# Kernel optimization log

Measured on AMD Instinct MI355X. Metric: run time of the kernel, lower is better.

Reference implementation:

```python
import jax, jax.numpy as jnp
import numpy as np


def _bilinear_resize_nchw(x, out_h, out_w):
    """Torch F.interpolate(mode='bilinear', align_corners=False), no antialias."""
    B, C, H, W = x.shape

    def coords(out_n, in_n):
        src = jnp.maximum(0.0, (jnp.arange(out_n, dtype=jnp.float32) + 0.5) * (in_n / out_n) - 0.5)
        f = jnp.floor(src)
        i0 = jnp.clip(f.astype(jnp.int32), 0, in_n - 1)
        i1 = jnp.clip(i0 + 1, 0, in_n - 1)
        frac = src - f
        return i0, i1, frac

    y0, y1, fy = coords(out_h, H)
    x0, x1, fx = coords(out_w, W)
    rows = x[:, :, y0, :] * (1.0 - fy)[None, None, :, None] + x[:, :, y1, :] * fy[None, None, :, None]
    out = rows[:, :, :, x0] * (1.0 - fx)[None, None, None, :] + rows[:, :, :, x1] * fx[None, None, None, :]
    return out


def setup_inputs() -> dict:
    key = jax.random.key(0)
    k1, k2, k3, k4 = jax.random.split(key, 4)
    return {
        "query_value": jax.random.normal(k1, (2, 256, 64, 128), dtype=jnp.float32),
        "memory_keys_low": jax.random.normal(k2, (2, 4, 64, 32, 64), dtype=jnp.float32),
        "memory_values_low": jax.random.normal(k3, (2, 4, 256, 32, 64), dtype=jnp.float32),
        "query_key_low": jax.random.normal(k4, (2, 64, 32, 64), dtype=jnp.float32),
    }


def reference(query_value, memory_keys_low, memory_values_low, query_key_low):
    B, T, Ck, H, W = memory_keys_low.shape
    Cv = memory_values_low.shape[2]
    # keys: BxTxCkxHxW -> Bx(T*H*W)xCk via permute(0,2,1,3,4)+view+permute
    mk = jnp.transpose(memory_keys_low, (0, 2, 1, 3, 4)).reshape(B, Ck, T * H * W)
    qk = query_key_low.reshape(B, Ck, H * W)
    # attn[b, m, n] over memory locations m (softmax axis), query locations n
    attn = jnp.einsum('bcm,bcn->bmn', mk, qk)  # [B, T*H*W, H*W]
    # matmul_norm=False: no key_channels**-0.5 scaling
    attn = jax.nn.softmax(attn, axis=1)
    mv = jnp.transpose(memory_values_low, (0, 2, 1, 3, 4)).reshape(B, Cv, T * H * W)
    memory = jnp.einsum('bcm,bmn->bcn', mv, attn).reshape(B, Cv, H, W)
    qv = _bilinear_resize_nchw(query_value, H, W)
    return jnp.concatenate([qv, memory], axis=1)  # [B, 2*Cv, H, W]
```

## Files before the change

kernel.cpp:

```cpp
#include <hip/hip_runtime.h>
#include <cstdint>

#define BATCH 2
#define TT    4
#define CKD   64
#define CVD   256
#define NQ    2048
#define MM    8192
#define TQ    64
#define TM    32
#define MSPLIT 8
#define MCHUNK (MM / MSPLIT)
#define NIT    (MCHUNK / TM)

typedef unsigned short u16;
typedef __bf16 bf16x8 __attribute__((ext_vector_type(8)));
typedef float  f32x4  __attribute__((ext_vector_type(4)));

struct __attribute__((aligned(8)))  U16x4 { u16 x, y, z, w; };
struct __attribute__((aligned(16))) U16x8 { u16 v[8]; };

__device__ __forceinline__ u16 f2bf(float x) {
    uint32_t u = __float_as_uint(x);
    uint32_t r = (u + 0x7FFFu + ((u >> 16) & 1u)) >> 16;
    return (u16)r;
}
__device__ __forceinline__ float bf2f(u16 h) {
    return __uint_as_float(((uint32_t)h) << 16);
}

#define MFMA(a, b, c) __builtin_amdgcn_mfma_f32_16x16x32_bf16((a), (b), (c), 0, 0, 0)

#define WS_VB   0u
#define WS_KHI  8388608u
#define WS_KLO  10485760u
#define WS_QHI  12582912u
#define WS_QLO  13107200u
#define WS_LP   13631488u
#define WS_UP   13893632u

__global__ __launch_bounds__(256)
void prep_fused(const float* __restrict__ qv, const float* __restrict__ mk,
                const float* __restrict__ qk, const float* __restrict__ mv,
                float* __restrict__ out, u16* __restrict__ vb,
                u16* __restrict__ khi, u16* __restrict__ klo,
                u16* __restrict__ qhi, u16* __restrict__ qlo) {
    const int bid = blockIdx.x;
    const int tid = threadIdx.x;

    if (bid < 4096) {
        int idx = bid * 256 + tid;
        int n  = idx & 2047;
        int bc = idx >> 11;
        int x = n & 63, y = n >> 6;
        const float* ib = qv + (size_t)bc * (64 * 128) + (2 * y) * 128 + 2 * x;
        float2 r0 = *(const float2*)ib;
        float2 r1 = *(const float2*)(ib + 128);
        int b = bc >> 8, c = bc & 255;
        out[((size_t)(b * 512 + c)) * NQ + n] = 0.25f * (r0.x + r0.y + r1.x + r1.y);
    } else if (bid < 6144) {
        int idx = (bid - 4096) * 256 + tid;
        const float4* s = (const float4*)mv + (size_t)idx * 2;
        float4 a = s[0], b = s[1];
        U16x8 o;
        o.v[0] = f2bf(a.x); o.v[1] = f2bf(a.y); o.v[2] = f2bf(a.z); o.v[3] = f2bf(a.w);
        o.v[4] = f2bf(b.x); o.v[5] = f2bf(b.y); o.v[6] = f2bf(b.z); o.v[7] = f2bf(b.w);
        *(U16x8*)(vb + (size_t)idx * 8) = o;
    } else {
        const float* src;
        u16 *dhi, *dlo;
        int blk;
        if (bid < 6656) { src = mk; dhi = khi; dlo = klo; blk = bid - 6144; }
        else            { src = qk; dhi = qhi; dlo = qlo; blk = bid - 6656; }
        int g  = blk >> 6;
        int mg = blk & 63;
        int c8 = (tid & 7) * 8;
        int m  = mg * 32 + (tid >> 3);
        const float* s = src + (size_t)g * 64 * 2048 + m;
        U16x8 hi, lo;
        #pragma unroll
        for (int j = 0; j < 8; ++j) {
            float v = s[(size_t)(c8 + j) * 2048];
            u16 h = f2bf(v);
            hi.v[j] = h;
            lo.v[j] = f2bf(v - bf2f(h));
        }
        size_t o = ((size_t)g * 2048 + m) * 64 + c8;
        *(U16x8*)(dhi + o) = hi;
        *(U16x8*)(dlo + o) = lo;
    }
}

__global__ __launch_bounds__(256, 2)
void flash_attn(const u16* __restrict__ khi_g, const u16* __restrict__ klo_g,
                const u16* __restrict__ vb_g, const u16* __restrict__ qhi_g,
                const u16* __restrict__ qlo_g, float* __restrict__ Up,
                float* __restrict__ Lp) {
    __shared__ __align__(16) u16 smem[2][17408];

    const int tid    = threadIdx.x;
    const int bx     = blockIdx.x;
    const int mchunk = bx & 7;
    const int ntile  = (bx >> 3) & 31;
    const int b      = bx >> 8;

    const int lane = tid & 63;
    const int w    = tid >> 6;
    const int quad = lane >> 4;
    const int l15  = lane & 15;

    const int bt      = b * TT + (mchunk >> 1);
    const int hw_base = (mchunk & 1) * MCHUNK;

    bf16x8 qh[2][2], ql[2][2];
    {
        const int nbase = ntile * TQ + (w >> 1) * 32;
        #pragma unroll
        for (int nsi = 0; nsi < 2; ++nsi) {
            size_t o = ((size_t)(b * NQ + nbase + nsi * 16 + l15)) * 64 + quad * 8;
            qh[nsi][0] = *(const bf16x8*)&qhi_g[o];
            qh[nsi][1] = *(const bf16x8*)&qhi_g[o + 32];
            ql[nsi][0] = *(const bf16x8*)&qlo_g[o];
            ql[nsi][1] = *(const bf16x8*)&qlo_g[o + 32];
        }
    }

    const u16* kh_base = khi_g + ((size_t)bt * 2048 + hw_base) * 64;
    const u16* kl_base = klo_g + ((size_t)bt * 2048 + hw_base) * 64;
    const u16* v_base  = vb_g + (size_t)bt * CVD * 2048 + hw_base;

    f32x4 O[2][8];
    #pragma unroll
    for (int i = 0; i < 2; ++i)
        #pragma unroll
        for (int j = 0; j < 8; ++j)
            O[i][j] = (f32x4){0.f, 0.f, 0.f, 0.f};
    float Lloc[2] = {0.f, 0.f};

    const int msub     = w & 1;
    const int nsubpair = w >> 1;
    const int npair    = w & 1;
    const int chalf    = w >> 1;

    const int km = tid >> 3;
    const int kc = (tid & 7) * 8;
    const int vc = tid >> 2;
    const int vm = (tid & 3) * 8;

    bf16x8 kh_r = *(const bf16x8*)&kh_base[(size_t)km * 64 + kc];
    bf16x8 kl_r = *(const bf16x8*)&kl_base[(size_t)km * 64 + kc];
    bf16x8 v_r[4];
    #pragma unroll
    for (int p = 0; p < 4; ++p)
        v_r[p] = *(const bf16x8*)&v_base[(size_t)(vc + p * 64) * 2048 + vm];

    #pragma unroll 2
    for (int it = 0; it < NIT; ++it) {
        u16* Khi = smem[it & 1];
        u16* Klo = Khi + 2304;
        u16* Vs  = Khi + 4608;
        u16* Ps  = Khi + 14848;

        *(bf16x8*)&Khi[km * 72 + kc] = kh_r;
        *(bf16x8*)&Klo[km * 72 + kc] = kl_r;
        #pragma unroll
        for (int p = 0; p < 4; ++p)
            *(bf16x8*)&Vs[(vc + p * 64) * 40 + vm] = v_r[p];

        if (it + 1 < NIT) {
            const int hw1 = (it + 1) * TM;
            kh_r = *(const bf16x8*)&kh_base[(size_t)(hw1 + km) * 64 + kc];
            kl_r = *(const bf16x8*)&kl_base[(size_t)(hw1 + km) * 64 + kc];
            #pragma unroll
            for (int p = 0; p < 4; ++p)
                v_r[p] = *(const bf16x8*)&v_base[(size_t)(vc + p * 64) * 2048 + hw1 + vm];
        }
        __syncthreads();

        f32x4 acc[2];
        acc[0] = (f32x4){0.f, 0.f, 0.f, 0.f};
        acc[1] = (f32x4){0.f, 0.f, 0.f, 0.f};
        #pragma unroll
        for (int ks = 0; ks < 2; ++ks) {
            bf16x8 ah = *(const bf16x8*)&Khi[(msub * 16 + l15) * 72 + ks * 32 + quad * 8];
            bf16x8 al = *(const bf16x8*)&Klo[(msub * 16 + l15) * 72 + ks * 32 + quad * 8];
            #pragma unroll
            for (int nsi = 0; nsi < 2; ++nsi) {
                acc[nsi] = MFMA(ah, qh[nsi][ks], acc[nsi]);
                acc[nsi] = MFMA(ah, ql[nsi][ks], acc[nsi]);
                acc[nsi] = MFMA(al, qh[nsi][ks], acc[nsi]);
            }
        }
        #pragma unroll
        for (int nsi = 0; nsi < 2; ++nsi) {
            int n = (nsubpair * 2 + nsi) * 16 + l15;
            float p0 = __expf(acc[nsi][0]);
            float p1 = __expf(acc[nsi][1]);
            float p2 = __expf(acc[nsi][2]);
            float p3 = __expf(acc[nsi][3]);
            Lloc[nsi] += (p0 + p1) + (p2 + p3);
            U16x4 pk = {f2bf(p0), f2bf(p1), f2bf(p2), f2bf(p3)};
            *(U16x4*)&Ps[n * 40 + msub * 16 + quad * 4] = pk;
        }
        __syncthreads();

        bf16x8 a2[2];
        #pragma unroll
        for (int nsi2 = 0; nsi2 < 2; ++nsi2)
            a2[nsi2] = *(const bf16x8*)&Ps[(npair * 32 + nsi2 * 16 + l15) * 40 + quad * 8];
        #pragma unroll
        for (int cs = 0; cs < 8; ++cs) {
            bf16x8 bv = *(const bf16x8*)&Vs[(chalf * 128 + cs * 16 + l15) * 40 + quad * 8];
            O[0][cs] = MFMA(a2[0], bv, O[0][cs]);
            O[1][cs] = MFMA(a2[1], bv, O[1][cs]);
        }
    }

    #pragma unroll
    for (int nsi = 0; nsi < 2; ++nsi) {
        float v = Lloc[nsi];
        v += __shfl_xor(v, 16);
        v += __shfl_xor(v, 32);
        if (quad == nsi) {
            int nsub = nsubpair * 2 + nsi;
            Lp[(((size_t)mchunk * 2 + msub) * BATCH + b) * NQ + ntile * TQ + nsub * 16 + l15] = v;
        }
    }

    float* ubase = Up + (((size_t)mchunk * BATCH + b) * NQ + ntile * TQ) * CVD
                 + (size_t)(npair * 32) * CVD + chalf * 128;
    #pragma unroll
    for (int nsi2 = 0; nsi2 < 2; ++nsi2) {
        #pragma unroll
        for (int cs = 0; cs < 8; ++cs) {
            #pragma unroll
            for (int r = 0; r < 4; ++r) {
                int n_local = nsi2 * 16 + quad * 4 + r;
                ubase[(size_t)n_local * CVD + cs * 16 + l15] = O[nsi2][cs][r];
            }
        }
    }
}

__global__ __launch_bounds__(256) void reduce_div(const float* __restrict__ Up,
                                                  const float* __restrict__ Lp,
                                                  float* __restrict__ out) {
    __shared__ float lds[16 * 257];
    const int tid = threadIdx.x;
    const int b   = blockIdx.x >> 7;
    const int n0  = (blockIdx.x & 127) * 16;

    float acc[16];
    #pragma unroll
    for (int j = 0; j < 16; ++j) acc[j] = 0.f;

    for (int ms = 0; ms < MSPLIT; ++ms) {
        const float* sb = Up + (((size_t)ms * BATCH + b) * NQ + n0) * CVD + tid * 16;
        #pragma unroll
        for (int k = 0; k < 4; ++k) {
            float4 v = *(const float4*)(sb + k * 4);
            acc[k * 4 + 0] += v.x; acc[k * 4 + 1] += v.y;
            acc[k * 4 + 2] += v.z; acc[k * 4 + 3] += v.w;
        }
    }

    const int n_local = tid >> 4;
    const int c0      = (tid & 15) * 16;
    float Lsum = 0.f;
    #pragma unroll
    for (int s = 0; s < MSPLIT * 2; ++s)
        Lsum += Lp[((size_t)s * BATCH + b) * NQ + n0 + n_local];
    const float inv = 1.0f / Lsum;

    #pragma unroll
    for (int j = 0; j < 16; ++j)
        lds[n_local * 257 + c0 + j] = acc[j] * inv;
    __syncthreads();

    float* ob = out + ((size_t)(b * 512 + 256 + tid)) * NQ + n0;
    #pragma unroll
    for (int k = 0; k < 4; ++k) {
        float4 v;
        v.x = lds[(4 * k + 0) * 257 + tid];
        v.y = lds[(4 * k + 1) * 257 + tid];
        v.z = lds[(4 * k + 2) * 257 + tid];
        v.w = lds[(4 * k + 3) * 257 + tid];
        *(float4*)(ob + 4 * k) = v;
    }
}

extern "C" void kernel_launch(void* const* d_in, const int* in_sizes, int n_in,
                              void* d_out, int out_size, void* d_ws, size_t ws_size,
                              hipStream_t stream) {
    const float* qv = (const float*)d_in[0];
    const float* mk = (const float*)d_in[1];
    const float* mv = (const float*)d_in[2];
    const float* qk = (const float*)d_in[3];
    float* out = (float*)d_out;

    u16*   vb  = (u16*)((char*)d_ws + WS_VB);
    u16*   khi = (u16*)((char*)d_ws + WS_KHI);
    u16*   klo = (u16*)((char*)d_ws + WS_KLO);
    u16*   qhi = (u16*)((char*)d_ws + WS_QHI);
    u16*   qlo = (u16*)((char*)d_ws + WS_QLO);
    float* Lp  = (float*)((char*)d_ws + WS_LP);
    float* Up  = (float*)((char*)d_ws + WS_UP);

    prep_fused<<<6784, 256, 0, stream>>>(qv, mk, qk, mv, out, vb, khi, klo, qhi, qlo);
    flash_attn<<<512, 256, 0, stream>>>(khi, klo, vb, qhi, qlo, Up, Lp);
    reduce_div<<<256, 256, 0, stream>>>(Up, Lp, out);
}
```

Before: 138.1 us.

## Shrink flash_attn LDS footprint and split reduce_div across channel quarters

In flash_attn, only the V tile stays double-buffered; the K hi/lo and P tiles become single buffers. The LDS row padding drops from 40 to 36, and the launch bound is raised to 3 blocks per CU, so more blocks can be resident. reduce_div is split into four channel quarters per 16-query tile, giving four times as many blocks with less work each. The new 72-byte LDS row stride breaks 16-byte alignment for the bf16x8 loads, which may split or slow those accesses. With only 512 flash_attn blocks, the higher occupancy limit may not raise residency at all.

```diff
diff --git a/kernel.cpp b/kernel.cpp
--- a/kernel.cpp
+++ b/kernel.cpp
@@ -38,6 +38,13 @@
 #define WS_QLO  13107200u
 #define WS_LP   13631488u
 #define WS_UP   13893632u
+
+#define LDS_KHI 0
+#define LDS_KLO 2304
+#define LDS_PS  4608
+#define LDS_VS  6912
+#define LDS_VSZ 9216
+#define LDS_TOT 25344
 
 __global__ __launch_bounds__(256)
 void prep_fused(const float* __restrict__ qv, const float* __restrict__ mk,
@@ -91,12 +98,15 @@
     }
 }
 
-__global__ __launch_bounds__(256, 2)
+__global__ __launch_bounds__(256, 3)
 void flash_attn(const u16* __restrict__ khi_g, const u16* __restrict__ klo_g,
                 const u16* __restrict__ vb_g, const u16* __restrict__ qhi_g,
                 const u16* __restrict__ qlo_g, float* __restrict__ Up,
                 float* __restrict__ Lp) {
-    __shared__ __align__(16) u16 smem[2][17408];
+    __shared__ __align__(16) u16 smem[LDS_TOT];
+    u16* Khi = smem + LDS_KHI;
+    u16* Klo = smem + LDS_KLO;
+    u16* Ps  = smem + LDS_PS;
 
     const int tid    = threadIdx.x;
     const int bx     = blockIdx.x;
@@ -156,16 +166,13 @@
 
     #pragma unroll 2
     for (int it = 0; it < NIT; ++it) {
-        u16* Khi = smem[it & 1];
-        u16* Klo = Khi + 2304;
-        u16* Vs  = Khi + 4608;
-        u16* Ps  = Khi + 14848;
+        u16* Vs = smem + LDS_VS + (it & 1) * LDS_VSZ;
 
         *(bf16x8*)&Khi[km * 72 + kc] = kh_r;
         *(bf16x8*)&Klo[km * 72 + kc] = kl_r;
         #pragma unroll
         for (int p = 0; p < 4; ++p)
-            *(bf16x8*)&Vs[(vc + p * 64) * 40 + vm] = v_r[p];
+            *(bf16x8*)&Vs[(vc + p * 64) * 36 + vm] = v_r[p];
 
         if (it + 1 < NIT) {
             const int hw1 = (it + 1) * TM;
@@ -200,17 +207,17 @@
             float p3 = __expf(acc[nsi][3]);
             Lloc[nsi] += (p0 + p1) + (p2 + p3);
             U16x4 pk = {f2bf(p0), f2bf(p1), f2bf(p2), f2bf(p3)};
-            *(U16x4*)&Ps[n * 40 + msub * 16 + quad * 4] = pk;
+            *(U16x4*)&Ps[n * 36 + msub * 16 + quad * 4] = pk;
         }
         __syncthreads();
 
         bf16x8 a2[2];
         #pragma unroll
         for (int nsi2 = 0; nsi2 < 2; ++nsi2)
-            a2[nsi2] = *(const bf16x8*)&Ps[(npair * 32 + nsi2 * 16 + l15) * 40 + quad * 8];
+            a2[nsi2] = *(const bf16x8*)&Ps[(npair * 32 + nsi2 * 16 + l15) * 36 + quad * 8];
         #pragma unroll
         for (int cs = 0; cs < 8; ++cs) {
-            bf16x8 bv = *(const bf16x8*)&Vs[(chalf * 128 + cs * 16 + l15) * 40 + quad * 8];
+            bf16x8 bv = *(const bf16x8*)&Vs[(chalf * 128 + cs * 16 + l15) * 36 + quad * 8];
             O[0][cs] = MFMA(a2[0], bv, O[0][cs]);
             O[1][cs] = MFMA(a2[1], bv, O[1][cs]);
         }
@@ -245,48 +252,42 @@
 __global__ __launch_bounds__(256) void reduce_div(const float* __restrict__ Up,
                                                   const float* __restrict__ Lp,
                                                   float* __restrict__ out) {
-    __shared__ float lds[16 * 257];
+    __shared__ float lds[16 * 65];
     const int tid = threadIdx.x;
-    const int b   = blockIdx.x >> 7;
-    const int n0  = (blockIdx.x & 127) * 16;
-
-    float acc[16];
-    #pragma unroll
-    for (int j = 0; j < 16; ++j) acc[j] = 0.f;
-
+    const int cq  = blockIdx.x & 3;
+    const int n0  = ((blockIdx.x >> 2) & 127) * 16;
+    const int b   = blockIdx.x >> 9;
+
+    const int n_local = tid >> 4;
+    const int c_loc   = (tid & 15) * 4;
+    const int c       = cq * 64 + c_loc;
+
+    float4 acc = {0.f, 0.f, 0.f, 0.f};
     for (int ms = 0; ms < MSPLIT; ++ms) {
-        const float* sb = Up + (((size_t)ms * BATCH + b) * NQ + n0) * CVD + tid * 16;
-        #pragma unroll
-        for (int k = 0; k < 4; ++k) {
-            float4 v = *(const float4*)(sb + k * 4);
-            acc[k * 4 + 0] += v.x; acc[k * 4 + 1] += v.y;
-            acc[k * 4 + 2] += v.z; acc[k * 4 + 3] += v.w;
-        }
-    }
-
-    const int n_local = tid >> 4;
-    const int c0      = (tid & 15) * 16;
+        float4 v = *(const float4*)(Up + (((size_t)ms * BATCH + b) * NQ + n0 + n_local) * CVD + c);
+        acc.x += v.x; acc.y += v.y; acc.z += v.z; acc.w += v.w;
+    }
+
     float Lsum = 0.f;
     #pragma unroll
     for (int s = 0; s < MSPLIT * 2; ++s)
         Lsum += Lp[((size_t)s * BATCH + b) * NQ + n0 + n_local];
     const float inv = 1.0f / Lsum;
 
-    #pragma unroll
-    for (int j = 0; j < 16; ++j)
-        lds[n_local * 257 + c0 + j] = acc[j] * inv;
+    lds[n_local * 65 + c_loc + 0] = acc.x * inv;
+    lds[n_local * 65 + c_loc + 1] = acc.y * inv;
+    lds[n_local * 65 + c_loc + 2] = acc.z * inv;
+    lds[n_local * 65 + c_loc + 3] = acc.w * inv;
     __syncthreads();
 
-    float* ob = out + ((size_t)(b * 512 + 256 + tid)) * NQ + n0;
-    #pragma unroll
-    for (int k = 0; k < 4; ++k) {
-        float4 v;
-        v.x = lds[(4 * k + 0) * 257 + tid];
-        v.y = lds[(4 * k + 1) * 257 + tid];
-        v.z = lds[(4 * k + 2) * 257 + tid];
-        v.w = lds[(4 * k + 3) * 257 + tid];
-        *(float4*)(ob + 4 * k) = v;
-    }
+    const int c_out = tid >> 2;
+    const int nq    = (tid & 3) * 4;
+    float4 v;
+    v.x = lds[(nq + 0) * 65 + c_out];
+    v.y = lds[(nq + 1) * 65 + c_out];
+    v.z = lds[(nq + 2) * 65 + c_out];
+    v.w = lds[(nq + 3) * 65 + c_out];
+    *(float4*)(out + ((size_t)(b * 512 + 256 + cq * 64 + c_out)) * NQ + n0 + nq) = v;
 }
 
 extern "C" void kernel_launch(void* const* d_in, const int* in_sizes, int n_in,
@@ -308,5 +309,5 @@
 
     prep_fused<<<6784, 256, 0, stream>>>(qv, mk, qk, mv, out, vb, khi, klo, qhi, qlo);
     flash_attn<<<512, 256, 0, stream>>>(khi, klo, vb, qhi, qlo, Up, Lp);
-    reduce_div<<<256, 256, 0, stream>>>(Up, Lp, out);
-}
+    reduce_div<<<1024, 256, 0, stream>>>(Up, Lp, out);
+}
```

Result: slower. 208.7 us (+51.1%).
